# Performance work log

Measured on AMD Instinct MI355X. Metric: run time of the kernel, lower is better.

Reference implementation:

```python
import jax, jax.numpy as jnp
import numpy as np

S, L, K = 4, 256, 32          # num_states, seq length, neighbors
ORIG_H, EMB_H, EXV, RANK = 128, 256, 384, 16


def _integrate(x, Wq, Wk, seq_idx, emb_idx, hidden, rank):
    """AttentionIntegrator.forward: QK^T softmax -> double mean -> softmax -> weighted pool of raw x."""
    x = jnp.moveaxis(x, (seq_idx, emb_idx), (-2, -1))
    orig_shape = x.shape
    Ls = orig_shape[-2]
    xf = x.reshape(-1, Ls, hidden)               # (B, Ls, hidden)
    B = xf.shape[0]
    q = (xf @ Wq.T).reshape(B, Ls, rank, hidden)  # head_dim == hidden
    k = (xf @ Wk.T).reshape(B, Ls, rank, hidden)
    scale = 1.0 / jnp.sqrt(jnp.asarray(hidden, xf.dtype))
    scores = jnp.einsum('blhd,bmhd->bhlm', q, k) * scale
    attn = jax.nn.softmax(scores, axis=-1)        # (B, rank, Ls, Ls)
    w = jax.nn.softmax(attn.mean(axis=(1, 2)), axis=-1)  # (B, Ls)
    pooled = jnp.einsum('bl,bld->bd', w, xf)      # (B, hidden)
    return (pooled.reshape(*orig_shape[:-2], hidden),
            w.reshape(*orig_shape[:-2], Ls))


def setup_inputs() -> dict:
    key = jax.random.key(0)
    ks = jax.random.split(key, 12)
    sc = lambda fan_in: 1.0 / np.sqrt(fan_in)
    return {
        'h_V':    jax.random.normal(ks[0], (S, L, ORIG_H), jnp.float32),
        'h_EXV':  jax.random.normal(ks[1], (S, L, K, EXV), jnp.float32),
        'W_hV':   jax.random.normal(ks[2], (EMB_H, ORIG_H), jnp.float32) * sc(ORIG_H),
        'b_hV':   jnp.zeros((EMB_H,), jnp.float32),
        'Wq_hv':  jax.random.normal(ks[3], (RANK * EMB_H, EMB_H), jnp.float32) * sc(EMB_H),
        'Wk_hv':  jax.random.normal(ks[4], (RANK * EMB_H, EMB_H), jnp.float32) * sc(EMB_H),
        'Wq_ce':  jax.random.normal(ks[5], (RANK * EXV, EXV), jnp.float32) * sc(EXV),
        'Wk_ce':  jax.random.normal(ks[6], (RANK * EXV, EXV), jnp.float32) * sc(EXV),
        'W_ce':   jax.random.normal(ks[7], (EMB_H, EXV), jnp.float32) * sc(EXV),
        'b_ce':   jnp.zeros((EMB_H,), jnp.float32),
        'Wq_sce': jax.random.normal(ks[8], (RANK * EMB_H, EMB_H), jnp.float32) * sc(EMB_H),
        'Wk_sce': jax.random.normal(ks[9], (RANK * EMB_H, EMB_H), jnp.float32) * sc(EMB_H),
    }


def reference(h_V, h_EXV, W_hV, b_hV, Wq_hv, Wk_hv, Wq_ce, Wk_ce, W_ce, b_ce, Wq_sce, Wk_sce):
    # diffmodel.get_weights
    hv = h_V @ W_hV.T + b_hV                                  # (S, L, EMB_H)
    h_V_int, h_V_w = _integrate(hv, Wq_hv, Wk_hv, 0, 2, EMB_H, RANK)   # pool over states
    # chemical environment: pool over k neighbors per (state, position)
    ce, _local_w = _integrate(h_EXV, Wq_ce, Wk_ce, 2, 3, EXV, RANK)    # (S, L, EXV)
    ce = ce @ W_ce.T + b_ce                                   # (S, L, EMB_H)
    ce_int, ce_w = _integrate(ce, Wq_sce, Wk_sce, 0, 2, EMB_H, RANK)   # pool over states
    return (h_V_int[None], h_V_w[None], ce_int[None], ce_w[None])
```

## Files before the change

### kernel.cpp

```cpp
#include <hip/hip_runtime.h>

typedef _Float16 f16;
typedef _Float16 f16x8 __attribute__((ext_vector_type(8)));
typedef _Float16 f16x4 __attribute__((ext_vector_type(4)));
typedef float f32x4 __attribute__((ext_vector_type(4)));

#define MFMA16(a, b, c) __builtin_amdgcn_mfma_f32_16x16x32_f16(a, b, c, 0, 0, 0)
#define MFMA16K16(a, b, c) __builtin_amdgcn_mfma_f32_16x16x16f16(a, b, c, 0, 0, 0)

__global__ __launch_bounds__(256) void k_mt(const float* __restrict__ Wq,
                                            const float* __restrict__ Wk,
                                            f16* __restrict__ MT, int H) {
    const int h = blockIdx.x;
    const int ntile = H >> 6;
    const int nkk = H >> 5;
    const int frow = (blockIdx.y / ntile) * 64;
    const int ecol = (blockIdx.y % ntile) * 64;
    const int t = threadIdx.x;
    const int lane = t & 63;
    const int w = t >> 6;
    const int wr = w >> 1, wc = w & 1;

    __shared__ __align__(16) f16 As[64][40];
    __shared__ __align__(16) f16 Ks[64][40];

    f32x4 acc[2][2] = {};
    const int d = t >> 3;
    const int e8 = (t & 7) * 8;

    for (int kk = 0; kk < nkk; ++kk) {
        const float* gq = Wq + (size_t)(h * H + kk * 32 + d) * H + ecol + e8;
        const float* gk = Wk + (size_t)(h * H + kk * 32 + d) * H + frow + e8;
        float q[8], k[8];
#pragma unroll
        for (int i = 0; i < 8; ++i) { q[i] = gq[i]; k[i] = gk[i]; }
        __syncthreads();
#pragma unroll
        for (int i = 0; i < 8; ++i) { As[e8 + i][d] = (f16)q[i]; Ks[e8 + i][d] = (f16)k[i]; }
        __syncthreads();
        f16x8 a[2], b[2];
#pragma unroll
        for (int rt = 0; rt < 2; ++rt)
            a[rt] = *(const f16x8*)&Ks[wr * 32 + rt * 16 + (lane & 15)][(lane >> 4) * 8];
#pragma unroll
        for (int nt = 0; nt < 2; ++nt)
            b[nt] = *(const f16x8*)&As[wc * 32 + nt * 16 + (lane & 15)][(lane >> 4) * 8];
#pragma unroll
        for (int rt = 0; rt < 2; ++rt)
#pragma unroll
            for (int nt = 0; nt < 2; ++nt)
                acc[rt][nt] = MFMA16(a[rt], b[nt], acc[rt][nt]);
    }
#pragma unroll
    for (int rt = 0; rt < 2; ++rt)
#pragma unroll
        for (int nt = 0; nt < 2; ++nt)
#pragma unroll
            for (int j = 0; j < 4; ++j) {
                int f = frow + wr * 32 + rt * 16 + (lane >> 4) * 4 + j;
                int e = ecol + wc * 32 + nt * 16 + (lane & 15);
                MT[(((size_t)h * nkk + (e >> 5)) * H + f) * 32 + (e & 31)] = (f16)acc[rt][nt][j];
            }
}

__global__ __launch_bounds__(256) void k_lin(const float* __restrict__ in,
                                             const float* __restrict__ W,
                                             const float* __restrict__ bias,
                                             float* __restrict__ out, int K) {
    const int t = threadIdx.x;
    const int r0 = blockIdx.x * 4;
    __shared__ float ins[4][384];
    __shared__ float Ws[256][33];
#pragma unroll
    for (int r = 0; r < 4; ++r)
        for (int off = t; off < K; off += 256)
            ins[r][off] = in[(size_t)(r0 + r) * K + off];
    float acc[4] = {};
    for (int d0 = 0; d0 < K; d0 += 32) {
        __syncthreads();
        for (int i = t; i < 256 * 32; i += 256) {
            int j = i >> 5, dd = i & 31;
            Ws[j][dd] = W[(size_t)j * K + d0 + dd];
        }
        __syncthreads();
#pragma unroll 8
        for (int dd = 0; dd < 32; ++dd) {
            float wv = Ws[t][dd];
#pragma unroll
            for (int r = 0; r < 4; ++r) acc[r] += wv * ins[r][d0 + dd];
        }
    }
    float bv = bias[t];
#pragma unroll
    for (int r = 0; r < 4; ++r) out[(size_t)(r0 + r) * 256 + t] = acc[r] + bv;
}

__global__ __launch_bounds__(256) void k_small_int(const float* __restrict__ X,
                                                   const f16* __restrict__ MT,
                                                   float* __restrict__ wpart) {
    const int t = threadIdx.x;
    const int lane = t & 63;
    const int w = t >> 6;
    const int g = lane >> 4;
    const int l15 = lane & 15;
    const int pos0 = blockIdx.x * 16;
    const int h = blockIdx.y;

    extern __shared__ __align__(16) char smem0[];
    f16(*Xs)[264] = (f16(*)[264])smem0;
    f16(*Ts)[264] = (f16(*)[264])(smem0 + 33792);

    {
        int row = t >> 2, d0 = (t & 3) * 64;
        int s = row & 3, p = row >> 2;
        const float* gx = X + (size_t)(s * 256 + pos0 + p) * 256 + d0;
#pragma unroll
        for (int i = 0; i < 8; ++i) {
            float4 v0 = *(const float4*)(gx + i * 8);
            float4 v1 = *(const float4*)(gx + i * 8 + 4);
            f16x8 o;
            o[0] = (f16)v0.x; o[1] = (f16)v0.y; o[2] = (f16)v0.z; o[3] = (f16)v0.w;
            o[4] = (f16)v1.x; o[5] = (f16)v1.y; o[6] = (f16)v1.z; o[7] = (f16)v1.w;
            *(f16x8*)&Xs[row][d0 + i * 8] = o;
        }
    }
    __syncthreads();

    const f16* mh = MT + (size_t)h * 8 * 256 * 32;
    const int fb = w * 64 + l15;
    f32x4 acc[4][4] = {};
    f16x8 bq[4], bn[4];
#pragma unroll
    for (int nt = 0; nt < 4; ++nt)
        bq[nt] = *(const f16x8*)(mh + (size_t)(fb + nt * 16) * 32 + g * 8);
#pragma unroll
    for (int kk = 0; kk < 8; ++kk) {
        if (kk < 7) {
#pragma unroll
            for (int nt = 0; nt < 4; ++nt)
                bn[nt] = *(const f16x8*)(mh + ((size_t)(kk + 1) * 256 + fb + nt * 16) * 32 + g * 8);
        }
        f16x8 a[4];
#pragma unroll
        for (int rt = 0; rt < 4; ++rt)
            a[rt] = *(const f16x8*)&Xs[rt * 16 + l15][kk * 32 + g * 8];
#pragma unroll
        for (int rt = 0; rt < 4; ++rt)
#pragma unroll
            for (int nt = 0; nt < 4; ++nt)
                acc[rt][nt] = MFMA16(a[rt], bq[nt], acc[rt][nt]);
#pragma unroll
        for (int nt = 0; nt < 4; ++nt) bq[nt] = bn[nt];
    }
#pragma unroll
    for (int rt = 0; rt < 4; ++rt)
#pragma unroll
        for (int nt = 0; nt < 4; ++nt)
#pragma unroll
            for (int j = 0; j < 4; ++j)
                Ts[rt * 16 + g * 4 + j][w * 64 + nt * 16 + l15] = (f16)acc[rt][nt][j];
    __syncthreads();

    f32x4 sacc = {};
#pragma unroll
    for (int ks = 0; ks < 8; ++ks) {
        f16x8 a = *(const f16x8*)&Ts[w * 16 + l15][ks * 32 + g * 8];
        f16x8 b = *(const f16x8*)&Xs[w * 16 + l15][ks * 32 + g * 8];
        sacc = MFMA16(a, b, sacc);
    }
    if ((l15 >> 2) == g) {
        const float scale = 1.0f / 16.0f;
        float add = 0.f;
#pragma unroll
        for (int j = 0; j < 4; ++j) {
            float v = sacc[j] * scale;
            float m = v;
            m = fmaxf(m, __shfl_xor(m, 1));
            m = fmaxf(m, __shfl_xor(m, 2));
            float e = expf(v - m);
            float s2 = e;
            s2 += __shfl_xor(s2, 1);
            s2 += __shfl_xor(s2, 2);
            add += e / s2;
        }
        int pg = pos0 + w * 4 + g;
        wpart[((size_t)h * 256 + pg) * 4 + (l15 & 3)] = add;
    }
}

__global__ __launch_bounds__(256) void k_small_fin(const float* __restrict__ wpart,
                                                   const float* __restrict__ X,
                                                   float* __restrict__ out_int,
                                                   float* __restrict__ out_w) {
    const int pos = blockIdx.x, t = threadIdx.x;
    __shared__ float red[64];
    __shared__ float ws[4];
    if (t < 64) red[t] = wpart[((size_t)(t >> 2) * 256 + pos) * 4 + (t & 3)];
    __syncthreads();
    if (t == 0) {
        float v[4];
#pragma unroll
        for (int s = 0; s < 4; ++s) {
            float x = 0.f;
            for (int hh = 0; hh < 16; ++hh) x += red[hh * 4 + s];
            v[s] = x * (1.0f / 64.0f);
        }
        float m = fmaxf(fmaxf(v[0], v[1]), fmaxf(v[2], v[3]));
        float sum = 0.f;
#pragma unroll
        for (int s = 0; s < 4; ++s) { v[s] = expf(v[s] - m); sum += v[s]; }
#pragma unroll
        for (int s = 0; s < 4; ++s) ws[s] = v[s] / sum;
    }
    __syncthreads();
    if (t < 4) out_w[pos * 4 + t] = ws[t];
    float v = 0.f;
#pragma unroll
    for (int s = 0; s < 4; ++s) v += ws[s] * X[(size_t)(s * 256 + pos) * 256 + t];
    out_int[(size_t)pos * 256 + t] = v;
}

#define PART_OFF 49152

__global__ __launch_bounds__(256, 2) void k_ce_int(const float* __restrict__ Xg32,
                                                   const f16* __restrict__ MT,
                                                   float* __restrict__ acc_out) {
    const int t = threadIdx.x;
    const int lane = t & 63;
    const int w = t >> 6;
    const int g = lane >> 4;
    const int l15 = lane & 15;
    const int bg = blockIdx.x;

    extern __shared__ __align__(16) char smem[];

    {
        const float* xg = Xg32 + (size_t)bg * 64 * 384;
#pragma unroll
        for (int p = 0; p < 12; ++p) {
            int idx = p * 256 + t;
            int row = idx / 48, s = idx - row * 48;
            int c = s ^ (row & 7);
            const float* src = xg + row * 384 + c * 8;
            float4 v0 = *(const float4*)src;
            float4 v1 = *(const float4*)(src + 4);
            f16x8 o;
            o[0] = (f16)v0.x; o[1] = (f16)v0.y; o[2] = (f16)v0.z; o[3] = (f16)v0.w;
            o[4] = (f16)v1.x; o[5] = (f16)v1.y; o[6] = (f16)v1.z; o[7] = (f16)v1.w;
            *(f16x8*)(smem + idx * 16) = o;
        }
    }
    __syncthreads();

    const f16* mall = MT;
    const int frow = w * 96 + l15;

    f16x8 aq[6], an[6];
#pragma unroll
    for (int ft = 0; ft < 6; ++ft)
        aq[ft] = *(const f16x8*)(mall + ((size_t)0 * 384 + frow + ft * 16) * 32 + g * 8);

    for (int hi = 0; hi < 16; ++hi) {
        f32x4 acc[6][4] = {};
#pragma unroll
        for (int kk = 0; kk < 12; ++kk) {
            int nstep = hi * 12 + kk + 1;
            if (nstep < 192) {
#pragma unroll
                for (int ft = 0; ft < 6; ++ft)
                    an[ft] = *(const f16x8*)(mall + ((size_t)nstep * 384 + frow + ft * 16) * 32 + g * 8);
            }
            f16x8 xb[4];
#pragma unroll
            for (int mt = 0; mt < 4; ++mt) {
                int row = mt * 16 + l15;
                int ch = kk * 4 + g;
                xb[mt] = *(const f16x8*)(smem + row * 768 + ((ch ^ (row & 7)) << 4));
            }
#pragma unroll
            for (int ft = 0; ft < 6; ++ft)
#pragma unroll
                for (int mt = 0; mt < 4; ++mt)
                    acc[ft][mt] = MFMA16(aq[ft], xb[mt], acc[ft][mt]);
#pragma unroll
            for (int ft = 0; ft < 6; ++ft) aq[ft] = an[ft];
        }

        f16x4 bf[6][4];
#pragma unroll
        for (int ft = 0; ft < 6; ++ft)
#pragma unroll
            for (int mt = 0; mt < 4; ++mt) {
                f32x4 v = acc[ft][mt];
                f16x4 o;
                o[0] = (f16)v[0]; o[1] = (f16)v[1]; o[2] = (f16)v[2]; o[3] = (f16)v[3];
                bf[ft][mt] = o;
            }

        f32x4 s2[2][2][2] = {};
#pragma unroll
        for (int b = 0; b < 2; ++b)
#pragma unroll
            for (int ks = 0; ks < 6; ++ks)
#pragma unroll
                for (int it = 0; it < 2; ++it) {
                    int r = b * 32 + it * 16 + l15;
                    int ch = 12 * w + 2 * ks + (g >> 1);
                    f16x4 av = *(const f16x4*)(smem + r * 768 + ((ch ^ (r & 7)) << 4) + 8 * (g & 1));
#pragma unroll
                    for (int lt = 0; lt < 2; ++lt)
                        s2[b][it][lt] = MFMA16K16(av, bf[ks][2 * b + lt], s2[b][it][lt]);
                }

#pragma unroll
        for (int b = 0; b < 2; ++b)
#pragma unroll
            for (int lt = 0; lt < 2; ++lt) {
                int dst = b * 2 + lt;
                if (dst != w) {
                    int src = w - (w > dst ? 1 : 0);
#pragma unroll
                    for (int it = 0; it < 2; ++it)
                        *(f32x4*)(smem + PART_OFF + (((dst * 3 + src) * 2 + it) << 10) + lane * 16) =
                            s2[b][it][lt];
                }
            }
        __syncthreads();

        {
            const int b = w >> 1, lt = w & 1;
            f32x4 own0, own1;
            if (w == 0)      { own0 = s2[0][0][0]; own1 = s2[0][1][0]; }
            else if (w == 1) { own0 = s2[0][0][1]; own1 = s2[0][1][1]; }
            else if (w == 2) { own0 = s2[1][0][0]; own1 = s2[1][1][0]; }
            else             { own0 = s2[1][0][1]; own1 = s2[1][1][1]; }
            f32x4 ssum[2] = { own0, own1 };
#pragma unroll
            for (int src = 0; src < 3; ++src)
#pragma unroll
                for (int it = 0; it < 2; ++it)
                    ssum[it] += *(const f32x4*)(smem + PART_OFF + (((w * 3 + src) * 2 + it) << 10) + lane * 16);

            const float scale = 0.051031036307982884f;
            float mx = -1e30f;
#pragma unroll
            for (int it = 0; it < 2; ++it)
#pragma unroll
                for (int j = 0; j < 4; ++j) mx = fmaxf(mx, ssum[it][j] * scale);
            mx = fmaxf(mx, __shfl_xor(mx, 16));
            mx = fmaxf(mx, __shfl_xor(mx, 32));
            float e[2][4];
            float den = 0.f;
#pragma unroll
            for (int it = 0; it < 2; ++it)
#pragma unroll
                for (int j = 0; j < 4; ++j) {
                    e[it][j] = expf(ssum[it][j] * scale - mx);
                    den += e[it][j];
                }
            den += __shfl_xor(den, 16);
            den += __shfl_xor(den, 32);
            float inv = 1.f / den;
            float cs[2][4];
#pragma unroll
            for (int it = 0; it < 2; ++it)
#pragma unroll
                for (int j = 0; j < 4; ++j) {
                    float v = e[it][j] * inv;
                    v += __shfl_xor(v, 1);
                    v += __shfl_xor(v, 2);
                    v += __shfl_xor(v, 4);
                    v += __shfl_xor(v, 8);
                    cs[it][j] = v;
                }
            if (l15 == 0) {
                float* o = acc_out + (((size_t)hi * 1024 + bg * 2 + b) * 2 + lt) * 32;
#pragma unroll
                for (int it = 0; it < 2; ++it)
#pragma unroll
                    for (int j = 0; j < 4; ++j)
                        o[it * 16 + g * 4 + j] = cs[it][j];
            }
        }
        __syncthreads();
    }
}

__global__ __launch_bounds__(128) void k_ce_pool(const float* __restrict__ accp,
                                                 const float* __restrict__ exv,
                                                 float* __restrict__ pooled) {
    const int b = blockIdx.x;
    const int t = threadIdx.x;
    __shared__ float wm[32];
    __shared__ float ww[32];
    if (t < 32) {
        float s = 0.f;
#pragma unroll
        for (int h = 0; h < 16; ++h) {
            s += accp[(((size_t)h * 1024 + b) * 2 + 0) * 32 + t];
            s += accp[(((size_t)h * 1024 + b) * 2 + 1) * 32 + t];
        }
        wm[t] = s * (1.0f / 512.0f);
    }
    __syncthreads();
    if (t == 0) {
        float m = wm[0];
        for (int i = 1; i < 32; ++i) m = fmaxf(m, wm[i]);
        float s = 0.f;
        for (int i = 0; i < 32; ++i) { float e = expf(wm[i] - m); ww[i] = e; s += e; }
        float inv = 1.f / s;
        for (int i = 0; i < 32; ++i) ww[i] *= inv;
    }
    __syncthreads();
    for (int d = t; d < 384; d += 128) {
        float v = 0.f;
#pragma unroll
        for (int m = 0; m < 32; ++m) v += ww[m] * exv[((size_t)b * 32 + m) * 384 + d];
        pooled[(size_t)b * 384 + d] = v;
    }
}

extern "C" void kernel_launch(void* const* d_in, const int* in_sizes, int n_in,
                              void* d_out, int out_size, void* d_ws, size_t ws_size,
                              hipStream_t stream) {
    const float* h_V    = (const float*)d_in[0];
    const float* h_EXV  = (const float*)d_in[1];
    const float* W_hV   = (const float*)d_in[2];
    const float* b_hV   = (const float*)d_in[3];
    const float* Wq_hv  = (const float*)d_in[4];
    const float* Wk_hv  = (const float*)d_in[5];
    const float* Wq_ce  = (const float*)d_in[6];
    const float* Wk_ce  = (const float*)d_in[7];
    const float* W_ce   = (const float*)d_in[8];
    const float* b_ce   = (const float*)d_in[9];
    const float* Wq_sce = (const float*)d_in[10];
    const float* Wk_sce = (const float*)d_in[11];
    float* out = (float*)d_out;

    char* ws = (char*)d_ws;
    f16*   mt_hv  = (f16*)(ws + 0);
    f16*   mt_sce = (f16*)(ws + 2097152);
    f16*   mt_ce  = (f16*)(ws + 4194304);
    float* hv     = (float*)(ws + 8912896);
    float* ce     = (float*)(ws + 9961472);
    float* accp   = (float*)(ws + 11010048);
    float* pooled = (float*)(ws + 15204352);
    float* wpart  = accp;

    k_mt<<<dim3(16, 16), 256, 0, stream>>>(Wq_hv, Wk_hv, mt_hv, 256);
    k_mt<<<dim3(16, 36), 256, 0, stream>>>(Wq_ce, Wk_ce, mt_ce, 384);
    k_mt<<<dim3(16, 16), 256, 0, stream>>>(Wq_sce, Wk_sce, mt_sce, 256);
    k_lin<<<256, 256, 0, stream>>>(h_V, W_hV, b_hV, hv, 128);
    k_small_int<<<dim3(16, 16), 256, 67584, stream>>>(hv, mt_hv, wpart);
    k_small_fin<<<256, 256, 0, stream>>>(wpart, hv, out + 0, out + 65536);
    k_ce_int<<<dim3(512), 256, 73728, stream>>>(h_EXV, mt_ce, accp);
    k_ce_pool<<<1024, 128, 0, stream>>>(accp, h_EXV, pooled);
    k_lin<<<256, 256, 0, stream>>>(pooled, W_ce, b_ce, ce, 384);
    k_small_int<<<dim3(16, 16), 256, 67584, stream>>>(ce, mt_sce, wpart);
    k_small_fin<<<256, 256, 0, stream>>>(wpart, ce, out + 66560, out + 132096);
}
```

Baseline: 328.9 us.

## Split small integrator into more blocks and deepen MT prefetch in ce kernel

k_small_int now handles 4 positions per block instead of 16, launching four times as many blocks with static shared memory so the small-state integration spreads across more CUs. Each block redundantly loads the full MT tiles for fewer rows, which raises global/L2 traffic for MT. In k_ce_int the MT fragment prefetch becomes a 3-slot ring buffer loading two steps ahead, and the MFMA block is wrapped in s_setprio to favour matrix issue. Together these aim to cut latency stalls, at the cost of more registers and more redundant MT reads.

```diff
diff --git a/kernel.cpp b/kernel.cpp
--- a/kernel.cpp
+++ b/kernel.cpp
@@ -103,32 +103,31 @@
     const int w = t >> 6;
     const int g = lane >> 4;
     const int l15 = lane & 15;
-    const int pos0 = blockIdx.x * 16;
+    const int pos0 = blockIdx.x * 4;
     const int h = blockIdx.y;
 
-    extern __shared__ __align__(16) char smem0[];
-    f16(*Xs)[264] = (f16(*)[264])smem0;
-    f16(*Ts)[264] = (f16(*)[264])(smem0 + 33792);
+    __shared__ __align__(16) f16 Xs[16][264];
+    __shared__ __align__(16) f16 Ts[16][264];
 
     {
-        int row = t >> 2, d0 = (t & 3) * 64;
+        int row = t >> 4, d0 = (t & 15) * 16;
         int s = row & 3, p = row >> 2;
         const float* gx = X + (size_t)(s * 256 + pos0 + p) * 256 + d0;
 #pragma unroll
-        for (int i = 0; i < 8; ++i) {
-            float4 v0 = *(const float4*)(gx + i * 8);
-            float4 v1 = *(const float4*)(gx + i * 8 + 4);
+        for (int i = 0; i < 16; i += 8) {
+            float4 v0 = *(const float4*)(gx + i);
+            float4 v1 = *(const float4*)(gx + i + 4);
             f16x8 o;
             o[0] = (f16)v0.x; o[1] = (f16)v0.y; o[2] = (f16)v0.z; o[3] = (f16)v0.w;
             o[4] = (f16)v1.x; o[5] = (f16)v1.y; o[6] = (f16)v1.z; o[7] = (f16)v1.w;
-            *(f16x8*)&Xs[row][d0 + i * 8] = o;
+            *(f16x8*)&Xs[row][d0 + i] = o;
         }
     }
     __syncthreads();
 
     const f16* mh = MT + (size_t)h * 8 * 256 * 32;
     const int fb = w * 64 + l15;
-    f32x4 acc[4][4] = {};
+    f32x4 acc[4] = {};
     f16x8 bq[4], bn[4];
 #pragma unroll
     for (int nt = 0; nt < 4; ++nt)
@@ -140,35 +139,27 @@
             for (int nt = 0; nt < 4; ++nt)
                 bn[nt] = *(const f16x8*)(mh + ((size_t)(kk + 1) * 256 + fb + nt * 16) * 32 + g * 8);
         }
-        f16x8 a[4];
-#pragma unroll
-        for (int rt = 0; rt < 4; ++rt)
-            a[rt] = *(const f16x8*)&Xs[rt * 16 + l15][kk * 32 + g * 8];
-#pragma unroll
-        for (int rt = 0; rt < 4; ++rt)
-#pragma unroll
-            for (int nt = 0; nt < 4; ++nt)
-                acc[rt][nt] = MFMA16(a[rt], bq[nt], acc[rt][nt]);
+        f16x8 a = *(const f16x8*)&Xs[l15][kk * 32 + g * 8];
+#pragma unroll
+        for (int nt = 0; nt < 4; ++nt) acc[nt] = MFMA16(a, bq[nt], acc[nt]);
 #pragma unroll
         for (int nt = 0; nt < 4; ++nt) bq[nt] = bn[nt];
     }
 #pragma unroll
-    for (int rt = 0; rt < 4; ++rt)
-#pragma unroll
-        for (int nt = 0; nt < 4; ++nt)
-#pragma unroll
-            for (int j = 0; j < 4; ++j)
-                Ts[rt * 16 + g * 4 + j][w * 64 + nt * 16 + l15] = (f16)acc[rt][nt][j];
+    for (int nt = 0; nt < 4; ++nt)
+#pragma unroll
+        for (int j = 0; j < 4; ++j)
+            Ts[g * 4 + j][w * 64 + nt * 16 + l15] = (f16)acc[nt][j];
     __syncthreads();
 
     f32x4 sacc = {};
 #pragma unroll
     for (int ks = 0; ks < 8; ++ks) {
-        f16x8 a = *(const f16x8*)&Ts[w * 16 + l15][ks * 32 + g * 8];
-        f16x8 b = *(const f16x8*)&Xs[w * 16 + l15][ks * 32 + g * 8];
+        f16x8 a = *(const f16x8*)&Ts[l15][ks * 32 + g * 8];
+        f16x8 b = *(const f16x8*)&Xs[l15][ks * 32 + g * 8];
         sacc = MFMA16(a, b, sacc);
     }
-    if ((l15 >> 2) == g) {
+    if (w == 0 && (l15 >> 2) == g) {
         const float scale = 1.0f / 16.0f;
         float add = 0.f;
 #pragma unroll
@@ -183,7 +174,7 @@
             s2 += __shfl_xor(s2, 2);
             add += e / s2;
         }
-        int pg = pos0 + w * 4 + g;
+        int pg = pos0 + g;
         wpart[((size_t)h * 256 + pg) * 4 + (l15 & 3)] = add;
     }
 }
@@ -255,20 +246,24 @@
     const f16* mall = MT;
     const int frow = w * 96 + l15;
 
-    f16x8 aq[6], an[6];
-#pragma unroll
-    for (int ft = 0; ft < 6; ++ft)
-        aq[ft] = *(const f16x8*)(mall + ((size_t)0 * 384 + frow + ft * 16) * 32 + g * 8);
+    f16x8 A[3][6];
+#pragma unroll
+    for (int ft = 0; ft < 6; ++ft) {
+        A[0][ft] = *(const f16x8*)(mall + ((size_t)0 * 384 + frow + ft * 16) * 32 + g * 8);
+        A[1][ft] = *(const f16x8*)(mall + ((size_t)1 * 384 + frow + ft * 16) * 32 + g * 8);
+    }
 
     for (int hi = 0; hi < 16; ++hi) {
         f32x4 acc[6][4] = {};
 #pragma unroll
         for (int kk = 0; kk < 12; ++kk) {
-            int nstep = hi * 12 + kk + 1;
-            if (nstep < 192) {
+            {
+                int step = hi * 12 + kk + 2;
+                int ns = step < 192 ? step : 191;
 #pragma unroll
                 for (int ft = 0; ft < 6; ++ft)
-                    an[ft] = *(const f16x8*)(mall + ((size_t)nstep * 384 + frow + ft * 16) * 32 + g * 8);
+                    A[(kk + 2) % 3][ft] =
+                        *(const f16x8*)(mall + ((size_t)ns * 384 + frow + ft * 16) * 32 + g * 8);
             }
             f16x8 xb[4];
 #pragma unroll
@@ -277,13 +272,13 @@
                 int ch = kk * 4 + g;
                 xb[mt] = *(const f16x8*)(smem + row * 768 + ((ch ^ (row & 7)) << 4));
             }
+            __builtin_amdgcn_s_setprio(1);
 #pragma unroll
             for (int ft = 0; ft < 6; ++ft)
 #pragma unroll
                 for (int mt = 0; mt < 4; ++mt)
-                    acc[ft][mt] = MFMA16(aq[ft], xb[mt], acc[ft][mt]);
-#pragma unroll
-            for (int ft = 0; ft < 6; ++ft) aq[ft] = an[ft];
+                    acc[ft][mt] = MFMA16(A[kk % 3][ft], xb[mt], acc[ft][mt]);
+            __builtin_amdgcn_s_setprio(0);
         }
 
         f16x4 bf[6][4];
@@ -451,11 +446,11 @@
     k_mt<<<dim3(16, 36), 256, 0, stream>>>(Wq_ce, Wk_ce, mt_ce, 384);
     k_mt<<<dim3(16, 16), 256, 0, stream>>>(Wq_sce, Wk_sce, mt_sce, 256);
     k_lin<<<256, 256, 0, stream>>>(h_V, W_hV, b_hV, hv, 128);
-    k_small_int<<<dim3(16, 16), 256, 67584, stream>>>(hv, mt_hv, wpart);
+    k_small_int<<<dim3(64, 16), 256, 0, stream>>>(hv, mt_hv, wpart);
     k_small_fin<<<256, 256, 0, stream>>>(wpart, hv, out + 0, out + 65536);
     k_ce_int<<<dim3(512), 256, 73728, stream>>>(h_EXV, mt_ce, accp);
     k_ce_pool<<<1024, 128, 0, stream>>>(accp, h_EXV, pooled);
     k_lin<<<256, 256, 0, stream>>>(pooled, W_ce, b_ce, ce, 384);
-    k_small_int<<<dim3(16, 16), 256, 67584, stream>>>(ce, mt_sce, wpart);
+    k_small_int<<<dim3(64, 16), 256, 0, stream>>>(ce, mt_sce, wpart);
     k_small_fin<<<256, 256, 0, stream>>>(wpart, ce, out + 66560, out + 132096);
 }
```

After: 315.3 us. 4.1% less time.
